# Optimization experiments

Measured on AMD Instinct MI355X. Metric: run time of the kernel, lower is better.

Reference implementation:

```python
import jax, jax.numpy as jnp
import numpy as np

ENC_H = 512
DEC_H = 1024

def setup_inputs() -> dict:
    key = jax.random.key(0)
    k1, k2, k3, k4 = jax.random.split(key, 4)
    B, S = 32, 2048
    s = jax.random.normal(k1, (B, DEC_H), dtype=jnp.float32)
    encoder_outputs = jax.random.normal(k2, (B, S, 2 * ENC_H), dtype=jnp.float32)
    # nn.Linear weights: attn: [dec_h, 2*enc_h + dec_h], v: [1, dec_h]
    fan_in_attn = 2 * ENC_H + DEC_H
    attn_w = jax.random.uniform(k3, (DEC_H, fan_in_attn), dtype=jnp.float32,
                                minval=-1.0, maxval=1.0) / np.sqrt(fan_in_attn)
    v_w = jax.random.uniform(k4, (1, DEC_H), dtype=jnp.float32,
                             minval=-1.0, maxval=1.0) / np.sqrt(DEC_H)
    return {"s": s, "encoder_outputs": encoder_outputs, "attn_w": attn_w, "v_w": v_w}

def reference(s, encoder_outputs, attn_w, v_w):
    # Split attn weight to avoid materializing the repeated/concatenated tensor:
    # cat([s_rep, enc], -1) @ W^T == s @ Ws^T (broadcast over S) + enc @ We^T
    W_s = attn_w[:, :DEC_H]            # [dec_h, dec_h] acts on s
    W_e = attn_w[:, DEC_H:]            # [dec_h, 2*enc_h] acts on encoder_outputs
    proj_s = jnp.einsum('bd,hd->bh', s, W_s)                   # [B, dec_h]
    proj_e = jnp.einsum('bse,he->bsh', encoder_outputs, W_e)   # [B, S, dec_h]
    energy = jnp.tanh(proj_s[:, None, :] + proj_e)             # [B, S, dec_h]
    scores = jnp.einsum('bsh,oh->bs', energy, v_w)             # [B, S]
    return jax.nn.softmax(scores, axis=1)
```

## Files before the change

### kernel.cpp

```cpp
#include <hip/hip_runtime.h>
#include <hip/hip_bf16.h>

#define KDIM 1024
#define HDIM 1024
#define BM   64
#define SPART 65536

typedef __attribute__((ext_vector_type(8))) short bf16x8_t;
typedef __attribute__((ext_vector_type(16))) float f32x16_t;
typedef __attribute__((ext_vector_type(4))) float f32x4_t;
typedef __attribute__((ext_vector_type(4))) unsigned int u32x4_t;
typedef __attribute__((ext_vector_type(2))) unsigned int u32x2_t;

__device__ __forceinline__ unsigned int pack2bf(float a, float b) {
    union { float f; unsigned int u; } ua, ub;
    ua.f = a; ub.f = b;
    unsigned int ra = (ua.u + 0x7fffu + ((ua.u >> 16) & 1u)) >> 16;
    unsigned int rb = (ub.u + 0x7fffu + ((ub.u >> 16) & 1u)) >> 16;
    return ra | (rb << 16);
}

__device__ __forceinline__ unsigned int cvtpk(float lo, float hi) {
    unsigned int r;
    asm("v_cvt_pk_bf16_f32 %0, %1, %2" : "=v"(r) : "v"(lo), "v"(hi));
    return r;
}

__global__ void cvt_we_k(const float* __restrict__ attn_w, unsigned short* __restrict__ we_t) {
    const int h = blockIdx.x;
    const int t = threadIdx.x;
    const f32x4_t v = *(const f32x4_t*)(attn_w + (size_t)h * 2048 + 1024 + (size_t)t * 4);
    u32x2_t o;
    o[0] = pack2bf(v[0], v[1]);
    o[1] = pack2bf(v[2], v[3]);
    const int ks  = t >> 2;
    const int e15 = (t & 3) * 4;
    *(u32x2_t*)&we_t[(size_t)ks * 16384 + h * 16 + e15] = o;
}

__global__ void proj_s_k(const float* __restrict__ s, const float* __restrict__ attn_w,
                         float* __restrict__ ps) {
    const int h = (blockIdx.x * blockDim.x + threadIdx.x) >> 6;
    const int lane = threadIdx.x & 63;
    const float* wr = attn_w + (size_t)h * 2048;
    float w[16];
#pragma unroll
    for (int i = 0; i < 16; ++i) w[i] = wr[lane + 64 * i];
    for (int b = 0; b < 32; ++b) {
        const float* sr = s + (size_t)b * 1024;
        float a = 0.f;
#pragma unroll
        for (int i = 0; i < 16; ++i) a = fmaf(w[i], sr[lane + 64 * i], a);
#pragma unroll
        for (int off = 32; off >= 1; off >>= 1) a += __shfl_xor(a, off, 64);
        if (lane == 0) ps[b * 1024 + h] = a;
    }
}

__launch_bounds__(512, 4)
__global__ void fused_main_k(const float* __restrict__ enc,
                             const unsigned short* __restrict__ we_t,
                             const float* __restrict__ ps,
                             const float* __restrict__ vw,
                             float* __restrict__ scores_part) {
    __shared__ unsigned short lds_a[2 * 64 * 128];

    const int t = threadIdx.x;
    const int bid = blockIdx.x;
    const int hhalf = bid & 1;
    const int rest = bid >> 1;
    const int m_swz = (rest & 7) * 128 + (rest >> 3);
    const int m_base = m_swz * BM;
    const int bidx = m_swz >> 5;

    const int lane = t & 63;
    const int wid  = t >> 6;
    const int l31  = lane & 31;
    const int h5   = lane >> 5;
    const int habs = hhalf * 512 + wid * 64;

    const int srow = t >> 4;
    const int sc8  = t & 15;

    auto stage_load_half = [&](int kc, int half, f32x4_t* r) {
        const int row = half * 32 + srow;
        const float* p = enc + (size_t)(m_base + row) * KDIM + kc * 128 + sc8 * 8;
        r[0] = *(const f32x4_t*)p;
        r[1] = *(const f32x4_t*)(p + 4);
    };
    auto stage_write_half = [&](int kc, int half, const f32x4_t* r) {
        const int slot = kc & 1;
        const int row = half * 32 + srow;
        u32x4_t pk;
        pk[0] = cvtpk(r[0][0], r[0][1]);
        pk[1] = cvtpk(r[0][2], r[0][3]);
        pk[2] = cvtpk(r[1][0], r[1][1]);
        pk[3] = cvtpk(r[1][2], r[1][3]);
        *(u32x4_t*)&lds_a[slot * 8192 + row * 128 + ((sc8 ^ (row & 15)) << 3)] = pk;
    };

    const unsigned short* btile = we_t + (size_t)(habs + l31) * 16 + h5 * 8;
    auto loadB = [&](int g, bf16x8_t* dst) {
        const unsigned short* bp = btile + (size_t)g * 16384;
        dst[0] = *(const bf16x8_t*)(bp);
        dst[1] = *(const bf16x8_t*)(bp + 512);
    };

    f32x16_t acc[2][2];
#pragma unroll
    for (int m = 0; m < 2; ++m)
#pragma unroll
        for (int nf = 0; nf < 2; ++nf)
#pragma unroll
            for (int r = 0; r < 16; ++r) acc[m][nf][r] = 0.f;

    bf16x8_t bbuf[4][2];
    f32x4_t rsA[2], rsB[2];

    loadB(0, bbuf[0]);
    loadB(1, bbuf[1]);
    loadB(2, bbuf[2]);
    stage_load_half(0, 0, rsA);
    stage_load_half(0, 1, rsB);
    stage_write_half(0, 0, rsA);
    stage_write_half(0, 1, rsB);
    __syncthreads();

#pragma unroll
    for (int g = 0; g < 64; ++g) {
        const int kc  = g >> 3;
        const int ksl = g & 7;

        if (g + 3 < 64) loadB(g + 3, bbuf[(g + 3) & 3]);
        if (ksl == 0 && kc < 7) stage_load_half(kc + 1, 0, rsA);
        if (ksl == 4 && kc < 7) stage_load_half(kc + 1, 1, rsB);

        const unsigned short* slotp = lds_a + (kc & 1) * 8192;
        const int ch = (((ksl << 1) + h5) ^ (l31 & 15)) << 3;
        const bf16x8_t a0 = *(const bf16x8_t*)&slotp[l31 * 128 + ch];
        const bf16x8_t a1 = *(const bf16x8_t*)&slotp[(32 + l31) * 128 + ch];
        const bf16x8_t* bfr = bbuf[g & 3];
        __builtin_amdgcn_s_setprio(1);
        acc[0][0] = __builtin_amdgcn_mfma_f32_32x32x16_bf16(a0, bfr[0], acc[0][0], 0, 0, 0);
        acc[1][0] = __builtin_amdgcn_mfma_f32_32x32x16_bf16(a1, bfr[0], acc[1][0], 0, 0, 0);
        acc[0][1] = __builtin_amdgcn_mfma_f32_32x32x16_bf16(a0, bfr[1], acc[0][1], 0, 0, 0);
        acc[1][1] = __builtin_amdgcn_mfma_f32_32x32x16_bf16(a1, bfr[1], acc[1][1], 0, 0, 0);
        __builtin_amdgcn_s_setprio(0);

        if (ksl == 3 && kc < 7) stage_write_half(kc + 1, 0, rsA);
        if (ksl == 7) {
            if (kc < 7) stage_write_half(kc + 1, 1, rsB);
            asm volatile("s_waitcnt lgkmcnt(0)" ::: "memory");
            __builtin_amdgcn_s_barrier();
        }
    }

    float sc2[2][16];
#pragma unroll
    for (int m = 0; m < 2; ++m)
#pragma unroll
        for (int r = 0; r < 16; ++r) sc2[m][r] = 0.f;

#pragma unroll
    for (int nf = 0; nf < 2; ++nf) {
        const int h = habs + nf * 32 + l31;
        const float pv = ps[bidx * 1024 + h];
        const float vv = vw[h];
#pragma unroll
        for (int m = 0; m < 2; ++m)
#pragma unroll
            for (int r = 0; r < 16; ++r) {
                const float x = acc[m][nf][r] + pv;
                const float e = __expf(2.0f * x);
                const float th = 1.0f - __fdividef(2.0f, e + 1.0f);
                sc2[m][r] = fmaf(vv, th, sc2[m][r]);
            }
    }

#pragma unroll
    for (int off = 1; off < 32; off <<= 1)
#pragma unroll
        for (int m = 0; m < 2; ++m)
#pragma unroll
            for (int r = 0; r < 16; ++r)
                sc2[m][r] += __shfl_xor(sc2[m][r], off, 64);

    __syncthreads();
    float* slds = (float*)lds_a;
    if (l31 == 0) {
#pragma unroll
        for (int m = 0; m < 2; ++m)
#pragma unroll
            for (int r = 0; r < 16; ++r) {
                const int row = m * 32 + (r & 3) + 8 * (r >> 2) + 4 * h5;
                slds[wid * 64 + row] = sc2[m][r];
            }
    }
    __syncthreads();
    if (t < 64) {
        float v = 0.f;
#pragma unroll
        for (int w = 0; w < 8; ++w) v += slds[w * 64 + t];
        scores_part[(size_t)hhalf * SPART + m_base + t] = v;
    }
}

__global__ void softmax_k(const float* __restrict__ sc, float* __restrict__ out) {
    const int b = blockIdx.x;
    const int t = threadIdx.x;
    const int lane = t & 63;
    const int w = t >> 6;
    const float* r0 = sc + (size_t)b * 2048;
    const float* r1 = sc + SPART + (size_t)b * 2048;
    float x[8];
#pragma unroll
    for (int i = 0; i < 8; ++i) x[i] = r0[i * 256 + t] + r1[i * 256 + t];
    float m = x[0];
#pragma unroll
    for (int i = 1; i < 8; ++i) m = fmaxf(m, x[i]);
#pragma unroll
    for (int off = 32; off >= 1; off >>= 1) m = fmaxf(m, __shfl_xor(m, off, 64));
    __shared__ float sred[4];
    __shared__ float sred2[4];
    if (lane == 0) sred[w] = m;
    __syncthreads();
    m = fmaxf(fmaxf(sred[0], sred[1]), fmaxf(sred[2], sred[3]));
    float ssum = 0.f;
#pragma unroll
    for (int i = 0; i < 8; ++i) { x[i] = expf(x[i] - m); ssum += x[i]; }
#pragma unroll
    for (int off = 32; off >= 1; off >>= 1) ssum += __shfl_xor(ssum, off, 64);
    if (lane == 0) sred2[w] = ssum;
    __syncthreads();
    const float inv = 1.0f / (sred2[0] + sred2[1] + sred2[2] + sred2[3]);
#pragma unroll
    for (int i = 0; i < 8; ++i) out[(size_t)b * 2048 + i * 256 + t] = x[i] * inv;
}

extern "C" void kernel_launch(void* const* d_in, const int* in_sizes, int n_in,
                              void* d_out, int out_size, void* d_ws, size_t ws_size,
                              hipStream_t stream) {
    const float* s      = (const float*)d_in[0];
    const float* enc    = (const float*)d_in[1];
    const float* attn_w = (const float*)d_in[2];
    const float* vw     = (const float*)d_in[3];
    float* out = (float*)d_out;

    unsigned short* we = (unsigned short*)d_ws;
    float* ps     = (float*)((char*)d_ws + (2u << 20));
    float* scores = (float*)((char*)d_ws + (2u << 20) + (128u << 10));

    cvt_we_k<<<1024, 256, 0, stream>>>(attn_w, we);
    proj_s_k<<<256, 256, 0, stream>>>(s, attn_w, ps);
    fused_main_k<<<2048, 512, 0, stream>>>(enc, we, ps, vw, scores);
    softmax_k<<<32, 256, 0, stream>>>(scores, out);
}
```

Before: 217.2 us.

## Pre-convert encoder outputs to swizzled bf16 and stream via direct-to-LDS loads

Adds a pass that converts the fp32 encoder outputs into a tiled, XOR-swizzled bf16 workspace copy. A new main kernel then streams these tiles into a 4-slot LDS ring using global_load_lds, with explicit vmcnt waits and B fragments prefetched into registers. This is meant to remove in-kernel fp32-to-bf16 conversion and halve the bytes the GEMM reads. In exchange it adds an extra full read and write pass over the encoder tensor and requires a large workspace, falling back to the old kernel if that workspace is unavailable.

```diff
diff --git a/kernel.cpp b/kernel.cpp
--- a/kernel.cpp
+++ b/kernel.cpp
@@ -11,6 +11,9 @@
 typedef __attribute__((ext_vector_type(4))) float f32x4_t;
 typedef __attribute__((ext_vector_type(4))) unsigned int u32x4_t;
 typedef __attribute__((ext_vector_type(2))) unsigned int u32x2_t;
+
+#define WAITVM(n) asm volatile("s_waitcnt vmcnt(" #n ")" ::: "memory")
+#define MEMFENCE() asm volatile("" ::: "memory")
 
 __device__ __forceinline__ unsigned int pack2bf(float a, float b) {
     union { float f; unsigned int u; } ua, ub;
@@ -24,6 +27,12 @@
     unsigned int r;
     asm("v_cvt_pk_bf16_f32 %0, %1, %2" : "=v"(r) : "v"(lo), "v"(hi));
     return r;
+}
+
+__device__ __forceinline__ void gload16(const void* g, void* l) {
+    __builtin_amdgcn_global_load_lds(
+        (const __attribute__((address_space(1))) void*)g,
+        (__attribute__((address_space(3))) void*)l, 16, 0, 0);
 }
 
 __global__ void cvt_we_k(const float* __restrict__ attn_w, unsigned short* __restrict__ we_t) {
@@ -54,6 +63,166 @@
 #pragma unroll
         for (int off = 32; off >= 1; off >>= 1) a += __shfl_xor(a, off, 64);
         if (lane == 0) ps[b * 1024 + h] = a;
+    }
+}
+
+__global__ void cvt_enc_k(const float* __restrict__ enc, unsigned short* __restrict__ enc16) {
+    const int bid = blockIdx.x;
+    const int mt = bid >> 3, kc = bid & 7;
+    const int t = threadIdx.x;
+#pragma unroll
+    for (int i = 0; i < 4; ++i) {
+        const int task = i * 256 + t;
+        const int row = task >> 4;
+        const int cw  = task & 15;
+        const float* p = enc + (size_t)(mt * 64 + row) * 1024 + kc * 128 + cw * 8;
+        const f32x4_t a = __builtin_nontemporal_load((const f32x4_t*)p);
+        const f32x4_t b = __builtin_nontemporal_load((const f32x4_t*)(p + 4));
+        u32x4_t pk;
+        pk[0] = cvtpk(a[0], a[1]);
+        pk[1] = cvtpk(a[2], a[3]);
+        pk[2] = cvtpk(b[0], b[1]);
+        pk[3] = cvtpk(b[2], b[3]);
+        *(u32x4_t*)&enc16[(size_t)bid * 8192 + row * 128 + ((cw ^ (row & 15)) << 3)] = pk;
+    }
+}
+
+__launch_bounds__(512, 4)
+__global__ void fused_main2_k(const unsigned short* __restrict__ enc16,
+                              const unsigned short* __restrict__ we_t,
+                              const float* __restrict__ ps,
+                              const float* __restrict__ vw,
+                              float* __restrict__ scores_part) {
+    __shared__ unsigned short lds_a[4 * 64 * 128];
+
+    const int t = threadIdx.x;
+    const int bid = blockIdx.x;
+    const int xcd   = bid & 7;
+    const int hhalf = (bid >> 3) & 1;
+    const int m_swz = xcd * 128 + (bid >> 4);
+    const int m_base = m_swz * BM;
+    const int bidx = m_swz >> 5;
+
+    const int lane = t & 63;
+    const int wid  = t >> 6;
+    const int l31  = lane & 31;
+    const int h5   = lane >> 5;
+    const int habs = hhalf * 512 + wid * 64;
+
+    const unsigned short* tile0 = enc16 + (size_t)m_swz * 65536;
+    char* ldsbyte = (char*)&lds_a[0];
+
+    auto stageG = [&](int kc) {
+        const unsigned short* g = tile0 + kc * 8192 + t * 8;
+        char* d = ldsbyte + (size_t)(kc & 3) * 16384 + wid * 1024;
+        gload16(g, d);
+        gload16(g + 4096, d + 8192);
+    };
+
+    const unsigned short* btile = we_t + (size_t)(habs + l31) * 16 + h5 * 8;
+    auto loadB = [&](int g, bf16x8_t* dst) {
+        const unsigned short* bp = btile + (size_t)g * 16384;
+        dst[0] = *(const bf16x8_t*)(bp);
+        dst[1] = *(const bf16x8_t*)(bp + 512);
+    };
+
+    f32x16_t acc[2][2];
+#pragma unroll
+    for (int m = 0; m < 2; ++m)
+#pragma unroll
+        for (int nf = 0; nf < 2; ++nf)
+#pragma unroll
+            for (int r = 0; r < 16; ++r) acc[m][nf][r] = 0.f;
+
+    bf16x8_t bbuf[4][2];
+
+    stageG(0);
+    stageG(1);
+    stageG(2);
+    MEMFENCE();
+    loadB(0, bbuf[0]);
+    loadB(1, bbuf[1]);
+    loadB(2, bbuf[2]);
+    WAITVM(10);
+    __builtin_amdgcn_s_barrier();
+
+#pragma unroll
+    for (int kc = 0; kc < 8; ++kc) {
+        const unsigned short* slotp = lds_a + (kc & 3) * 8192;
+#pragma unroll
+        for (int ksl = 0; ksl < 8; ++ksl) {
+            const int g = kc * 8 + ksl;
+            if (g + 3 < 64) loadB(g + 3, bbuf[(g + 3) & 3]);
+            const int ch = (((ksl << 1) + h5) ^ (l31 & 15)) << 3;
+            const bf16x8_t a0 = *(const bf16x8_t*)&slotp[l31 * 128 + ch];
+            const bf16x8_t a1 = *(const bf16x8_t*)&slotp[(32 + l31) * 128 + ch];
+            const bf16x8_t* bfr = bbuf[g & 3];
+            __builtin_amdgcn_s_setprio(1);
+            acc[0][0] = __builtin_amdgcn_mfma_f32_32x32x16_bf16(a0, bfr[0], acc[0][0], 0, 0, 0);
+            acc[1][0] = __builtin_amdgcn_mfma_f32_32x32x16_bf16(a1, bfr[0], acc[1][0], 0, 0, 0);
+            acc[0][1] = __builtin_amdgcn_mfma_f32_32x32x16_bf16(a0, bfr[1], acc[0][1], 0, 0, 0);
+            acc[1][1] = __builtin_amdgcn_mfma_f32_32x32x16_bf16(a1, bfr[1], acc[1][1], 0, 0, 0);
+            __builtin_amdgcn_s_setprio(0);
+        }
+        MEMFENCE();
+        if (kc + 3 < 8) stageG(kc + 3);
+        if (kc < 7) {
+            if      (kc == 0) WAITVM(26);
+            else if (kc == 1) WAITVM(42);
+            else if (kc == 5) WAITVM(34);
+            else if (kc == 6) WAITVM(32);
+            else              WAITVM(36);
+            __builtin_amdgcn_s_barrier();
+        }
+    }
+
+    float sc2[2][16];
+#pragma unroll
+    for (int m = 0; m < 2; ++m)
+#pragma unroll
+        for (int r = 0; r < 16; ++r) sc2[m][r] = 0.f;
+
+#pragma unroll
+    for (int nf = 0; nf < 2; ++nf) {
+        const int h = habs + nf * 32 + l31;
+        const float pv = ps[bidx * 1024 + h];
+        const float vv = vw[h];
+#pragma unroll
+        for (int m = 0; m < 2; ++m)
+#pragma unroll
+            for (int r = 0; r < 16; ++r) {
+                const float x = acc[m][nf][r] + pv;
+                const float e = __expf(2.0f * x);
+                const float th = 1.0f - __fdividef(2.0f, e + 1.0f);
+                sc2[m][r] = fmaf(vv, th, sc2[m][r]);
+            }
+    }
+
+#pragma unroll
+    for (int off = 1; off < 32; off <<= 1)
+#pragma unroll
+        for (int m = 0; m < 2; ++m)
+#pragma unroll
+            for (int r = 0; r < 16; ++r)
+                sc2[m][r] += __shfl_xor(sc2[m][r], off, 64);
+
+    __syncthreads();
+    float* slds = (float*)lds_a;
+    if (l31 == 0) {
+#pragma unroll
+        for (int m = 0; m < 2; ++m)
+#pragma unroll
+            for (int r = 0; r < 16; ++r) {
+                const int row = m * 32 + (r & 3) + 8 * (r >> 2) + 4 * h5;
+                slds[wid * 64 + row] = sc2[m][r];
+            }
+    }
+    __syncthreads();
+    if (t < 64) {
+        float v = 0.f;
+#pragma unroll
+        for (int w = 0; w < 8; ++w) v += slds[w * 64 + t];
+        scores_part[(size_t)hhalf * SPART + m_base + t] = v;
     }
 }
 
@@ -249,9 +418,17 @@
     unsigned short* we = (unsigned short*)d_ws;
     float* ps     = (float*)((char*)d_ws + (2u << 20));
     float* scores = (float*)((char*)d_ws + (2u << 20) + (128u << 10));
+    unsigned short* enc16 = (unsigned short*)((char*)d_ws + (4u << 20));
+
+    const size_t need = (4ull << 20) + (128ull << 20);
 
     cvt_we_k<<<1024, 256, 0, stream>>>(attn_w, we);
     proj_s_k<<<256, 256, 0, stream>>>(s, attn_w, ps);
-    fused_main_k<<<2048, 512, 0, stream>>>(enc, we, ps, vw, scores);
+    if (ws_size >= need) {
+        cvt_enc_k<<<8192, 256, 0, stream>>>(enc, enc16);
+        fused_main2_k<<<2048, 512, 0, stream>>>(enc16, we, ps, vw, scores);
+    } else {
+        fused_main_k<<<2048, 512, 0, stream>>>(enc, we, ps, vw, scores);
+    }
     softmax_k<<<32, 256, 0, stream>>>(scores, out);
 }
```

Result: slower. 248.1 us (+14.2%).

## Stage encoder tiles via direct global-to-LDS loads with fp32 buffering and bf16 conversion at read

Applied to the files above, without the earlier changes.

Encoder fp32 tiles are now copied straight from global memory into LDS with global_load_lds, which removes the per-thread register staging and the convert-then-write step. The conversion to bf16 moves to the LDS read side, just before each MFMA. A 4-slot ring with two chunks in flight is kept in order with explicit vmcnt waits and barriers. The block-to-XCD swizzle is also changed. This doubles LDS traffic per element and adds conversion work inside the MFMA loop, and the hand-tuned vmcnt counts are fragile.

```diff
diff --git a/kernel.cpp b/kernel.cpp
--- a/kernel.cpp
+++ b/kernel.cpp
@@ -11,6 +11,9 @@
 typedef __attribute__((ext_vector_type(4))) float f32x4_t;
 typedef __attribute__((ext_vector_type(4))) unsigned int u32x4_t;
 typedef __attribute__((ext_vector_type(2))) unsigned int u32x2_t;
+
+#define WAITVM(n) asm volatile("s_waitcnt vmcnt(" #n ")" ::: "memory")
+#define MEMFENCE() asm volatile("" ::: "memory")
 
 __device__ __forceinline__ unsigned int pack2bf(float a, float b) {
     union { float f; unsigned int u; } ua, ub;
@@ -24,6 +27,12 @@
     unsigned int r;
     asm("v_cvt_pk_bf16_f32 %0, %1, %2" : "=v"(r) : "v"(lo), "v"(hi));
     return r;
+}
+
+__device__ __forceinline__ void gload16(const void* g, void* l) {
+    __builtin_amdgcn_global_load_lds(
+        (const __attribute__((address_space(1))) void*)g,
+        (__attribute__((address_space(3))) void*)l, 16, 0, 0);
 }
 
 __global__ void cvt_we_k(const float* __restrict__ attn_w, unsigned short* __restrict__ we_t) {
@@ -58,18 +67,18 @@
 }
 
 __launch_bounds__(512, 4)
-__global__ void fused_main_k(const float* __restrict__ enc,
-                             const unsigned short* __restrict__ we_t,
-                             const float* __restrict__ ps,
-                             const float* __restrict__ vw,
-                             float* __restrict__ scores_part) {
-    __shared__ unsigned short lds_a[2 * 64 * 128];
+__global__ void fused_main3_k(const float* __restrict__ enc,
+                              const unsigned short* __restrict__ we_t,
+                              const float* __restrict__ ps,
+                              const float* __restrict__ vw,
+                              float* __restrict__ scores_part) {
+    __shared__ float lds_a[4 * 64 * 64];
 
     const int t = threadIdx.x;
     const int bid = blockIdx.x;
-    const int hhalf = bid & 1;
-    const int rest = bid >> 1;
-    const int m_swz = (rest & 7) * 128 + (rest >> 3);
+    const int xcd   = bid & 7;
+    const int hhalf = (bid >> 3) & 1;
+    const int m_swz = xcd * 128 + (bid >> 4);
     const int m_base = m_swz * BM;
     const int bidx = m_swz >> 5;
 
@@ -79,24 +88,17 @@
     const int h5   = lane >> 5;
     const int habs = hhalf * 512 + wid * 64;
 
-    const int srow = t >> 4;
-    const int sc8  = t & 15;
-
-    auto stage_load_half = [&](int kc, int half, f32x4_t* r) {
-        const int row = half * 32 + srow;
-        const float* p = enc + (size_t)(m_base + row) * KDIM + kc * 128 + sc8 * 8;
-        r[0] = *(const f32x4_t*)p;
-        r[1] = *(const f32x4_t*)(p + 4);
-    };
-    auto stage_write_half = [&](int kc, int half, const f32x4_t* r) {
-        const int slot = kc & 1;
-        const int row = half * 32 + srow;
-        u32x4_t pk;
-        pk[0] = cvtpk(r[0][0], r[0][1]);
-        pk[1] = cvtpk(r[0][2], r[0][3]);
-        pk[2] = cvtpk(r[1][0], r[1][1]);
-        pk[3] = cvtpk(r[1][2], r[1][3]);
-        *(u32x4_t*)&lds_a[slot * 8192 + row * 128 + ((sc8 ^ (row & 15)) << 3)] = pk;
+    const int gr = t >> 4;
+    const int gc = (t & 15) ^ (gr & 15);
+    const float* gbase0 = enc + (size_t)(m_base + gr) * KDIM + gc * 4;
+    const float* gbase1 = gbase0 + (size_t)32 * KDIM;
+
+    auto stageG = [&](int kc) {
+        const float* g0 = gbase0 + kc * 64;
+        const float* g1 = gbase1 + kc * 64;
+        char* d = (char*)lds_a + (kc & 3) * 16384 + t * 16;
+        gload16(g0, d);
+        gload16(g1, d + 8192);
     };
 
     const unsigned short* btile = we_t + (size_t)(habs + l31) * 16 + h5 * 8;
@@ -115,43 +117,58 @@
             for (int r = 0; r < 16; ++r) acc[m][nf][r] = 0.f;
 
     bf16x8_t bbuf[4][2];
-    f32x4_t rsA[2], rsB[2];
-
+
+    stageG(0);
+    stageG(1);
+    MEMFENCE();
     loadB(0, bbuf[0]);
     loadB(1, bbuf[1]);
     loadB(2, bbuf[2]);
-    stage_load_half(0, 0, rsA);
-    stage_load_half(0, 1, rsB);
-    stage_write_half(0, 0, rsA);
-    stage_write_half(0, 1, rsB);
-    __syncthreads();
-
-#pragma unroll
-    for (int g = 0; g < 64; ++g) {
-        const int kc  = g >> 3;
-        const int ksl = g & 7;
-
-        if (g + 3 < 64) loadB(g + 3, bbuf[(g + 3) & 3]);
-        if (ksl == 0 && kc < 7) stage_load_half(kc + 1, 0, rsA);
-        if (ksl == 4 && kc < 7) stage_load_half(kc + 1, 1, rsB);
-
-        const unsigned short* slotp = lds_a + (kc & 1) * 8192;
-        const int ch = (((ksl << 1) + h5) ^ (l31 & 15)) << 3;
-        const bf16x8_t a0 = *(const bf16x8_t*)&slotp[l31 * 128 + ch];
-        const bf16x8_t a1 = *(const bf16x8_t*)&slotp[(32 + l31) * 128 + ch];
-        const bf16x8_t* bfr = bbuf[g & 3];
-        __builtin_amdgcn_s_setprio(1);
-        acc[0][0] = __builtin_amdgcn_mfma_f32_32x32x16_bf16(a0, bfr[0], acc[0][0], 0, 0, 0);
-        acc[1][0] = __builtin_amdgcn_mfma_f32_32x32x16_bf16(a1, bfr[0], acc[1][0], 0, 0, 0);
-        acc[0][1] = __builtin_amdgcn_mfma_f32_32x32x16_bf16(a0, bfr[1], acc[0][1], 0, 0, 0);
-        acc[1][1] = __builtin_amdgcn_mfma_f32_32x32x16_bf16(a1, bfr[1], acc[1][1], 0, 0, 0);
-        __builtin_amdgcn_s_setprio(0);
-
-        if (ksl == 3 && kc < 7) stage_write_half(kc + 1, 0, rsA);
-        if (ksl == 7) {
-            if (kc < 7) stage_write_half(kc + 1, 1, rsB);
-            asm volatile("s_waitcnt lgkmcnt(0)" ::: "memory");
+    WAITVM(8);
+    __builtin_amdgcn_s_barrier();
+    MEMFENCE();
+
+    const int xr = l31 & 15;
+    const int a0base = l31 * 256;
+    const int a1base = (32 + l31) * 256;
+
+#pragma unroll
+    for (int kc = 0; kc < 16; ++kc) {
+        const char* slotp = (const char*)lds_a + (kc & 3) * 16384;
+#pragma unroll
+        for (int ksl = 0; ksl < 4; ++ksl) {
+            const int g = kc * 4 + ksl;
+            if (g + 3 < 64) loadB(g + 3, bbuf[(g + 3) & 3]);
+
+            const int co = (((ksl << 2) + (h5 << 1)) ^ xr) << 4;
+            const f32x4_t lo0 = *(const f32x4_t*)(slotp + a0base + co);
+            const f32x4_t hi0 = *(const f32x4_t*)(slotp + a0base + (co ^ 16));
+            const f32x4_t lo1 = *(const f32x4_t*)(slotp + a1base + co);
+            const f32x4_t hi1 = *(const f32x4_t*)(slotp + a1base + (co ^ 16));
+            union { u32x4_t u; bf16x8_t b; } ca0, ca1;
+            ca0.u[0] = cvtpk(lo0[0], lo0[1]);
+            ca0.u[1] = cvtpk(lo0[2], lo0[3]);
+            ca0.u[2] = cvtpk(hi0[0], hi0[1]);
+            ca0.u[3] = cvtpk(hi0[2], hi0[3]);
+            ca1.u[0] = cvtpk(lo1[0], lo1[1]);
+            ca1.u[1] = cvtpk(lo1[2], lo1[3]);
+            ca1.u[2] = cvtpk(hi1[0], hi1[1]);
+            ca1.u[3] = cvtpk(hi1[2], hi1[3]);
+
+            const bf16x8_t* bfr = bbuf[g & 3];
+            __builtin_amdgcn_s_setprio(1);
+            acc[0][0] = __builtin_amdgcn_mfma_f32_32x32x16_bf16(ca0.b, bfr[0], acc[0][0], 0, 0, 0);
+            acc[1][0] = __builtin_amdgcn_mfma_f32_32x32x16_bf16(ca1.b, bfr[0], acc[1][0], 0, 0, 0);
+            acc[0][1] = __builtin_amdgcn_mfma_f32_32x32x16_bf16(ca0.b, bfr[1], acc[0][1], 0, 0, 0);
+            acc[1][1] = __builtin_amdgcn_mfma_f32_32x32x16_bf16(ca1.b, bfr[1], acc[1][1], 0, 0, 0);
+            __builtin_amdgcn_s_setprio(0);
+        }
+        MEMFENCE();
+        if (kc + 2 < 16) stageG(kc + 2);
+        if (kc < 15) {
+            if (kc == 14) WAITVM(8); else WAITVM(10);
             __builtin_amdgcn_s_barrier();
+            MEMFENCE();
         }
     }
 
@@ -252,6 +269,6 @@
 
     cvt_we_k<<<1024, 256, 0, stream>>>(attn_w, we);
     proj_s_k<<<256, 256, 0, stream>>>(s, attn_w, ps);
-    fused_main_k<<<2048, 512, 0, stream>>>(enc, we, ps, vw, scores);
+    fused_main3_k<<<2048, 512, 0, stream>>>(enc, we, ps, vw, scores);
     softmax_k<<<32, 256, 0, stream>>>(scores, out);
 }
```

New measurement: 269.2 us. 1.24x slower.
